# Kernel optimization log

Measured on AMD Instinct MI355X. Metric: run time of the kernel, lower is better.

The kernel has to match this reference:

```python
import jax, jax.numpy as jnp
import numpy as np

B = 1_048_576
NUM_ITERS = 10  # training-mode default; eval mode uses 1000
EPS = 1e-12
LOW, HIGH = 0.02, 0.98  # SquashedSigmoid bounds


def setup_inputs() -> dict:
    key = jax.random.key(0)
    ks = jax.random.split(key, 4)
    # margins are population masses -> keep strictly positive
    margins = jax.random.uniform(ks[0], (B, 8), dtype=jnp.float32) + 0.1

    def lin(k, i, o):
        return (jax.random.normal(k, (i, o), jnp.float32) / np.sqrt(i)).astype(jnp.float32)

    return {
        "margins": margins,
        "W1": lin(ks[1], 8, 32), "b1": jnp.zeros((32,), jnp.float32),
        "W2": lin(ks[2], 32, 16), "b2": jnp.zeros((16,), jnp.float32),
        "W3": lin(ks[3], 16, 9), "b3": jnp.zeros((9,), jnp.float32),
    }


def tau_batched(p):
    # p: (B,4) positive params -> (B,3,3) positive couples matrix.
    # 2x2 core, extended by geometric-mean row/col (user-supplied tau in repo).
    a = p.reshape(-1, 2, 2)
    col3 = jnp.sqrt(a[:, :, 0] * a[:, :, 1])          # (B,2)
    row3 = jnp.sqrt(a[:, 0, :] * a[:, 1, :])          # (B,2)
    corner = jnp.sqrt(row3[:, 0] * row3[:, 1])        # (B,)
    top = jnp.concatenate([a, col3[:, :, None]], axis=2)                 # (B,2,3)
    bot = jnp.concatenate([row3, corner[:, None]], axis=1)[:, None, :]   # (B,1,3)
    return jnp.concatenate([top, bot], axis=1)        # (B,3,3)


def sinkhorn_knopp(A, row_margins, col_margins, iters):
    # Batched Sinkhorn-Knopp: A (B,R,C), row_margins (B,R), col_margins (B,C)
    r = row_margins[:, :, None]
    c = col_margins[:, None, :]

    def body(A, _):
        A = A * (r / (A.sum(axis=2, keepdims=True) + EPS))
        A = A * (c / (A.sum(axis=1, keepdims=True) + EPS))
        return A, None

    A, _ = jax.lax.scan(body, A, None, length=iters)
    return A


def reference(margins, W1, b1, W2, b2, W3, b3):
    Bn = margins.shape[0]
    M, F = margins[:, 0:3], margins[:, 3:6]

    # MLP: Linear-ReLU-Linear-ReLU-Linear
    h = jax.nn.relu(margins @ W1 + b1)
    h = jax.nn.relu(h @ W2 + b2)
    pars = h @ W3 + b3                                   # (B,9)

    muc = tau_batched(jnp.exp(pars[:, 0:4]))             # (B,3,3)
    sqs = lambda x: LOW + (HIGH - LOW) * jax.nn.sigmoid(x)
    shm, shf = sqs(pars[:, 4:6]), sqs(pars[:, 6:8])      # (B,2) each
    V = jnp.exp(pars[:, -1])                             # (B,)

    ones = jnp.ones((Bn, 1), margins.dtype)
    shm0 = jnp.concatenate([shm, ones], axis=1)          # (B,3)
    shf0 = jnp.concatenate([shf, ones], axis=1)          # (B,3)
    mucm0, muc0f = M * shm0, F * shf0                    # matched masses (margins)
    mum0, mu0f = M * (1.0 - shm0), F * (1.0 - shf0)      # singles

    muc = sinkhorn_knopp(muc, mucm0, muc0f, NUM_ITERS)   # (B,3,3)

    top = jnp.concatenate([muc, mum0[:, :, None]], axis=2)   # (B,3,4)
    bot = jnp.concatenate(
        [mu0f[:, None, :], jnp.zeros((Bn, 1, 1), margins.dtype)], axis=2)  # (B,1,4)
    mus = jnp.concatenate([top, bot], axis=1)            # (B,4,4)
    return mus, V
```

## Files before the change

kernel.cpp:

```cpp
#include <hip/hip_runtime.h>
#include <math.h>


#define QLOW  0.02f
#define QSPAN 0.96f
#define L2E   1.44269504088896f

constexpr int R = 2;

typedef __attribute__((ext_vector_type(2))) float f32x2;

__device__ __forceinline__ float frcp(float x) { return __builtin_amdgcn_rcpf(x); }
__device__ __forceinline__ f32x2 pfma(f32x2 a, f32x2 b, f32x2 c) {
    return __builtin_elementwise_fma(a, b, c);
}

__global__ __launch_bounds__(256) void sinkhorn_fused(
    const float* __restrict__ margins,
    const float* __restrict__ W1, const float* __restrict__ b1,
    const float* __restrict__ W2, const float* __restrict__ b2,
    const float* __restrict__ W3, const float* __restrict__ b3,
    float* __restrict__ out, int n)
{
    const int tid  = blockIdx.x * blockDim.x + threadIdx.x;
    const int lane = tid & 63;
    const int base = (tid >> 6) * (64 * R) + lane;

    const float4* __restrict__ m4 = (const float4*)margins;

    float m[R][8];
#pragma unroll
    for (int r = 0; r < R; ++r) {
        const int row = base + 64 * r;
        const float4 a0 = m4[row * 2 + 0];
        const float4 a1 = m4[row * 2 + 1];
        m[r][0] = a0.x; m[r][1] = a0.y; m[r][2] = a0.z; m[r][3] = a0.w;
        m[r][4] = a1.x; m[r][5] = a1.y; m[r][6] = a1.z; m[r][7] = a1.w;
    }

    const f32x2* __restrict__ W1v = (const f32x2*)W1;
    const f32x2* __restrict__ W2v = (const f32x2*)W2;
    const f32x2* __restrict__ b1v = (const f32x2*)b1;
    const f32x2* __restrict__ b2v = (const f32x2*)b2;

    f32x2 h1[R][16];
#pragma unroll
    for (int j = 0; j < 16; ++j) {
        const f32x2 bb = b1v[j];
#pragma unroll
        for (int r = 0; r < R; ++r) h1[r][j] = bb;
    }
#pragma unroll
    for (int k = 0; k < 8; ++k) {
        f32x2 mk[R];
#pragma unroll
        for (int r = 0; r < R; ++r) { mk[r].x = m[r][k]; mk[r].y = m[r][k]; }
#pragma unroll
        for (int j = 0; j < 16; ++j) {
            const f32x2 w = W1v[k * 16 + j];
#pragma unroll
            for (int r = 0; r < R; ++r) h1[r][j] = pfma(mk[r], w, h1[r][j]);
        }
    }
    const f32x2 zero2 = {0.0f, 0.0f};
#pragma unroll
    for (int j = 0; j < 16; ++j)
#pragma unroll
        for (int r = 0; r < R; ++r)
            h1[r][j] = __builtin_elementwise_max(h1[r][j], zero2);

    f32x2 h2[R][8];
#pragma unroll
    for (int j = 0; j < 8; ++j) {
        const f32x2 bb = b2v[j];
#pragma unroll
        for (int r = 0; r < R; ++r) h2[r][j] = bb;
    }
#pragma unroll
    for (int k = 0; k < 32; ++k) {
        f32x2 hk[R];
#pragma unroll
        for (int r = 0; r < R; ++r) {
            const float s = (k & 1) ? h1[r][k >> 1].y : h1[r][k >> 1].x;
            hk[r].x = s; hk[r].y = s;
        }
#pragma unroll
        for (int j = 0; j < 8; ++j) {
            const f32x2 w = W2v[k * 8 + j];
#pragma unroll
            for (int r = 0; r < R; ++r) h2[r][j] = pfma(hk[r], w, h2[r][j]);
        }
    }
#pragma unroll
    for (int j = 0; j < 8; ++j)
#pragma unroll
        for (int r = 0; r < R; ++r)
            h2[r][j] = __builtin_elementwise_max(h2[r][j], zero2);

    f32x2 p01[R], p23[R], p45[R], p67[R];
    float p8[R];
    {
        const f32x2 b01 = {b3[0], b3[1]};
        const f32x2 b23 = {b3[2], b3[3]};
        const f32x2 b45 = {b3[4], b3[5]};
        const f32x2 b67 = {b3[6], b3[7]};
        const float b8  = b3[8];
#pragma unroll
        for (int r = 0; r < R; ++r) {
            p01[r] = b01; p23[r] = b23; p45[r] = b45; p67[r] = b67; p8[r] = b8;
        }
    }
#pragma unroll
    for (int k = 0; k < 16; ++k) {
        const f32x2 w01 = {W3[k * 9 + 0], W3[k * 9 + 1]};
        const f32x2 w23 = {W3[k * 9 + 2], W3[k * 9 + 3]};
        const f32x2 w45 = {W3[k * 9 + 4], W3[k * 9 + 5]};
        const f32x2 w67 = {W3[k * 9 + 6], W3[k * 9 + 7]};
        const float w8  = W3[k * 9 + 8];
#pragma unroll
        for (int r = 0; r < R; ++r) {
            const float s = (k & 1) ? h2[r][k >> 1].y : h2[r][k >> 1].x;
            f32x2 hb; hb.x = s; hb.y = s;
            p01[r] = pfma(hb, w01, p01[r]);
            p23[r] = pfma(hb, w23, p23[r]);
            p45[r] = pfma(hb, w45, p45[r]);
            p67[r] = pfma(hb, w67, p67[r]);
            p8[r]  = fmaf(s, w8, p8[r]);
        }
    }

    float4* __restrict__ o4 = (float4*)out;
    float* __restrict__ oV = out + (size_t)n * 16;

#pragma unroll
    for (int r = 0; r < R; ++r) {
        const int row = base + 64 * r;

        const float l0 = p01[r].x * L2E, l1 = p01[r].y * L2E;
        const float l2 = p23[r].x * L2E, l3 = p23[r].y * L2E;

        const float a00 = exp2f(l0), a01 = exp2f(l1);
        const float a10 = exp2f(l2), a11 = exp2f(l3);
        const float h01 = (l0 + l1) * 0.5f, h23 = (l2 + l3) * 0.5f;
        const float a02 = exp2f(h01);
        const float a12 = exp2f(h23);
        const float a20 = exp2f((l0 + l2) * 0.5f);
        const float a21 = exp2f((l1 + l3) * 0.5f);
        const float a22 = exp2f((h01 + h23) * 0.5f);

        const float s4 = fmaf(QSPAN, frcp(1.0f + exp2f(-L2E * p45[r].x)), QLOW);
        const float s5 = fmaf(QSPAN, frcp(1.0f + exp2f(-L2E * p45[r].y)), QLOW);
        const float s6 = fmaf(QSPAN, frcp(1.0f + exp2f(-L2E * p67[r].x)), QLOW);
        const float s7 = fmaf(QSPAN, frcp(1.0f + exp2f(-L2E * p67[r].y)), QLOW);

        const float M0 = m[r][0], M1 = m[r][1], M2 = m[r][2];
        const float F0 = m[r][3], F1 = m[r][4], F2 = m[r][5];

        const float rm0 = M0 * s4, rm1 = M1 * s5, rm2 = M2;
        const float cm0 = F0 * s6, cm1 = F1 * s7, cm2 = F2;
        const float um0 = fmaf(-s4, M0, M0);
        const float um1 = fmaf(-s5, M1, M1);
        const float uf0 = fmaf(-s6, F0, F0);
        const float uf1 = fmaf(-s7, F1, F1);

        const float B00 = a00 * rm0, B01 = a01 * rm0, B02 = a02 * rm0;
        const float B10 = a10 * rm1, B11 = a11 * rm1, B12 = a12 * rm1;
        const float B20 = a20 * rm2, B21 = a21 * rm2, B22 = a22 * rm2;
        const float C00 = a00 * cm0, C01 = a01 * cm1, C02 = a02 * cm2;
        const float C10 = a10 * cm0, C11 = a11 * cm1, C12 = a12 * cm2;
        const float C20 = a20 * cm0, C21 = a21 * cm1, C22 = a22 * cm2;

        float t0 = (a00 + a01) + a02;
        float t1 = (a10 + a11) + a12;
        float t2 = (a20 + a21) + a22;
        float z0, z1, z2, w0, w1, w2;
#pragma unroll
        for (int it = 0; it < 10; ++it) {
            z0 = frcp(t0); z1 = frcp(t1); z2 = frcp(t2);
            const float q0 = fmaf(B20, z2, fmaf(B10, z1, B00 * z0));
            const float q1 = fmaf(B21, z2, fmaf(B11, z1, B01 * z0));
            const float q2 = fmaf(B22, z2, fmaf(B12, z1, B02 * z0));
            w0 = frcp(q0); w1 = frcp(q1); w2 = frcp(q2);
            if (it < 9) {
                t0 = fmaf(C02, w2, fmaf(C01, w1, C00 * w0));
                t1 = fmaf(C12, w2, fmaf(C11, w1, C10 * w0));
                t2 = fmaf(C22, w2, fmaf(C21, w1, C20 * w0));
            }
        }
        const float u0 = rm0 * z0, u1 = rm1 * z1, u2 = rm2 * z2;
        const float v0 = cm0 * w0, v1 = cm1 * w1, v2 = cm2 * w2;

        const float A0f = u0 * a00 * v0, A1f = u0 * a01 * v1, A2f = u0 * a02 * v2;
        const float A3f = u1 * a10 * v0, A4f = u1 * a11 * v1, A5f = u1 * a12 * v2;
        const float A6f = u2 * a20 * v0, A7f = u2 * a21 * v1, A8f = u2 * a22 * v2;

        o4[row * 4 + 0] = make_float4(A0f, A1f, A2f, um0);
        o4[row * 4 + 1] = make_float4(A3f, A4f, A5f, um1);
        o4[row * 4 + 2] = make_float4(A6f, A7f, A8f, 0.0f);
        o4[row * 4 + 3] = make_float4(uf0, uf1, 0.0f, 0.0f);
        oV[row] = exp2f(p8[r] * L2E);
    }
}

extern "C" void kernel_launch(void* const* d_in, const int* in_sizes, int n_in,
                              void* d_out, int out_size, void* d_ws, size_t ws_size,
                              hipStream_t stream) {
    const float* margins = (const float*)d_in[0];
    const float* W1 = (const float*)d_in[1];
    const float* b1 = (const float*)d_in[2];
    const float* W2 = (const float*)d_in[3];
    const float* b2 = (const float*)d_in[4];
    const float* W3 = (const float*)d_in[5];
    const float* b3 = (const float*)d_in[6];

    const int n = in_sizes[0] / 8;
    const int threads = n / R;
    dim3 block(256), grid(threads / 256);

    sinkhorn_fused<<<grid, block, 0, stream>>>(margins, W1, b1, W2, b2, W3, b3,
                                               (float*)d_out, n);
}
```

Measured before the change: 126.5 us.

## Stage MLP weights in LDS and process one row per thread

Each block now copies W1, W2, W3 and the biases into shared memory, with W3 padded to 12-wide rows so it can be read with float4 LDS loads. The two-rows-per-thread register tiling is dropped in favour of one row per thread, which doubles the grid and lowers register pressure to raise occupancy. The final product also reuses the precomputed C coefficients instead of recomputing v. This trades scalar or global loads of uniform weights for LDS broadcast reads plus a barrier, and gives up the reuse of each weight load across two rows.

```diff
diff --git a/kernel.cpp b/kernel.cpp
--- a/kernel.cpp
+++ b/kernel.cpp
@@ -5,8 +5,6 @@
 #define QLOW  0.02f
 #define QSPAN 0.96f
 #define L2E   1.44269504088896f
-
-constexpr int R = 2;
 
 typedef __attribute__((ext_vector_type(2))) float f32x2;
 
@@ -22,184 +20,160 @@
     const float* __restrict__ W3, const float* __restrict__ b3,
     float* __restrict__ out, int n)
 {
-    const int tid  = blockIdx.x * blockDim.x + threadIdx.x;
-    const int lane = tid & 63;
-    const int base = (tid >> 6) * (64 * R) + lane;
+    __shared__ __align__(16) float sW1[256];
+    __shared__ __align__(16) float sW2[512];
+    __shared__ __align__(16) float sW3[16 * 12];
+    __shared__ __align__(16) float sB1[32];
+    __shared__ __align__(16) float sB2[16];
+    __shared__ __align__(16) float sB3[12];
+
+    {
+        const int t = threadIdx.x;
+        sW1[t] = W1[t];
+        sW2[t] = W2[t];
+        sW2[t + 256] = W2[t + 256];
+        if (t < 144) { const int k = t / 9, j = t - 9 * k; sW3[k * 12 + j] = W3[t]; }
+        if (t < 32) sB1[t] = b1[t];
+        if (t < 16) sB2[t] = b2[t];
+        if (t < 9)  sB3[t] = b3[t];
+    }
+    __syncthreads();
+
+    const float4* __restrict__ sW1q = (const float4*)sW1;
+    const float4* __restrict__ sW2q = (const float4*)sW2;
+    const float4* __restrict__ sW3q = (const float4*)sW3;
+
+    const int row = blockIdx.x * blockDim.x + threadIdx.x;
 
     const float4* __restrict__ m4 = (const float4*)margins;
+    const float4 a0 = m4[row * 2 + 0];
+    const float4 a1 = m4[row * 2 + 1];
+    float m[8];
+    m[0] = a0.x; m[1] = a0.y; m[2] = a0.z; m[3] = a0.w;
+    m[4] = a1.x; m[5] = a1.y; m[6] = a1.z; m[7] = a1.w;
 
-    float m[R][8];
+    f32x2 h1[16];
 #pragma unroll
-    for (int r = 0; r < R; ++r) {
-        const int row = base + 64 * r;
-        const float4 a0 = m4[row * 2 + 0];
-        const float4 a1 = m4[row * 2 + 1];
-        m[r][0] = a0.x; m[r][1] = a0.y; m[r][2] = a0.z; m[r][3] = a0.w;
-        m[r][4] = a1.x; m[r][5] = a1.y; m[r][6] = a1.z; m[r][7] = a1.w;
-    }
-
-    const f32x2* __restrict__ W1v = (const f32x2*)W1;
-    const f32x2* __restrict__ W2v = (const f32x2*)W2;
-    const f32x2* __restrict__ b1v = (const f32x2*)b1;
-    const f32x2* __restrict__ b2v = (const f32x2*)b2;
-
-    f32x2 h1[R][16];
-#pragma unroll
-    for (int j = 0; j < 16; ++j) {
-        const f32x2 bb = b1v[j];
-#pragma unroll
-        for (int r = 0; r < R; ++r) h1[r][j] = bb;
-    }
+    for (int j = 0; j < 16; ++j) { h1[j].x = sB1[2 * j]; h1[j].y = sB1[2 * j + 1]; }
 #pragma unroll
     for (int k = 0; k < 8; ++k) {
-        f32x2 mk[R];
+        f32x2 mk; mk.x = m[k]; mk.y = m[k];
 #pragma unroll
-        for (int r = 0; r < R; ++r) { mk[r].x = m[r][k]; mk[r].y = m[r][k]; }
-#pragma unroll
-        for (int j = 0; j < 16; ++j) {
-            const f32x2 w = W1v[k * 16 + j];
-#pragma unroll
-            for (int r = 0; r < R; ++r) h1[r][j] = pfma(mk[r], w, h1[r][j]);
+        for (int j4 = 0; j4 < 8; ++j4) {
+            const float4 w = sW1q[k * 8 + j4];
+            const f32x2 wa = {w.x, w.y};
+            const f32x2 wb = {w.z, w.w};
+            h1[2 * j4 + 0] = pfma(mk, wa, h1[2 * j4 + 0]);
+            h1[2 * j4 + 1] = pfma(mk, wb, h1[2 * j4 + 1]);
         }
     }
     const f32x2 zero2 = {0.0f, 0.0f};
 #pragma unroll
-    for (int j = 0; j < 16; ++j)
+    for (int j = 0; j < 16; ++j) h1[j] = __builtin_elementwise_max(h1[j], zero2);
+
+    f32x2 h2[8];
 #pragma unroll
-        for (int r = 0; r < R; ++r)
-            h1[r][j] = __builtin_elementwise_max(h1[r][j], zero2);
-
-    f32x2 h2[R][8];
-#pragma unroll
-    for (int j = 0; j < 8; ++j) {
-        const f32x2 bb = b2v[j];
-#pragma unroll
-        for (int r = 0; r < R; ++r) h2[r][j] = bb;
-    }
+    for (int j = 0; j < 8; ++j) { h2[j].x = sB2[2 * j]; h2[j].y = sB2[2 * j + 1]; }
 #pragma unroll
     for (int k = 0; k < 32; ++k) {
-        f32x2 hk[R];
+        const float s = (k & 1) ? h1[k >> 1].y : h1[k >> 1].x;
+        f32x2 hk; hk.x = s; hk.y = s;
 #pragma unroll
-        for (int r = 0; r < R; ++r) {
-            const float s = (k & 1) ? h1[r][k >> 1].y : h1[r][k >> 1].x;
-            hk[r].x = s; hk[r].y = s;
-        }
-#pragma unroll
-        for (int j = 0; j < 8; ++j) {
-            const f32x2 w = W2v[k * 8 + j];
-#pragma unroll
-            for (int r = 0; r < R; ++r) h2[r][j] = pfma(hk[r], w, h2[r][j]);
+        for (int j4 = 0; j4 < 4; ++j4) {
+            const float4 w = sW2q[k * 4 + j4];
+            const f32x2 wa = {w.x, w.y};
+            const f32x2 wb = {w.z, w.w};
+            h2[2 * j4 + 0] = pfma(hk, wa, h2[2 * j4 + 0]);
+            h2[2 * j4 + 1] = pfma(hk, wb, h2[2 * j4 + 1]);
         }
     }
 #pragma unroll
-    for (int j = 0; j < 8; ++j)
+    for (int j = 0; j < 8; ++j) h2[j] = __builtin_elementwise_max(h2[j], zero2);
+
+    f32x2 p01 = {sB3[0], sB3[1]};
+    f32x2 p23 = {sB3[2], sB3[3]};
+    f32x2 p45 = {sB3[4], sB3[5]};
+    f32x2 p67 = {sB3[6], sB3[7]};
+    float p8 = sB3[8];
 #pragma unroll
-        for (int r = 0; r < R; ++r)
-            h2[r][j] = __builtin_elementwise_max(h2[r][j], zero2);
+    for (int k = 0; k < 16; ++k) {
+        const float4 wA = sW3q[k * 3 + 0];
+        const float4 wB = sW3q[k * 3 + 1];
+        const float w8  = sW3[k * 12 + 8];
+        const float s = (k & 1) ? h2[k >> 1].y : h2[k >> 1].x;
+        f32x2 hb; hb.x = s; hb.y = s;
+        p01 = pfma(hb, (f32x2){wA.x, wA.y}, p01);
+        p23 = pfma(hb, (f32x2){wA.z, wA.w}, p23);
+        p45 = pfma(hb, (f32x2){wB.x, wB.y}, p45);
+        p67 = pfma(hb, (f32x2){wB.z, wB.w}, p67);
+        p8  = fmaf(s, w8, p8);
+    }
 
-    f32x2 p01[R], p23[R], p45[R], p67[R];
-    float p8[R];
-    {
-        const f32x2 b01 = {b3[0], b3[1]};
-        const f32x2 b23 = {b3[2], b3[3]};
-        const f32x2 b45 = {b3[4], b3[5]};
-        const f32x2 b67 = {b3[6], b3[7]};
-        const float b8  = b3[8];
+    const float l0 = p01.x * L2E, l1 = p01.y * L2E;
+    const float l2 = p23.x * L2E, l3 = p23.y * L2E;
+
+    const float a00 = exp2f(l0), a01 = exp2f(l1);
+    const float a10 = exp2f(l2), a11 = exp2f(l3);
+    const float h01 = (l0 + l1) * 0.5f, h23 = (l2 + l3) * 0.5f;
+    const float a02 = exp2f(h01);
+    const float a12 = exp2f(h23);
+    const float a20 = exp2f((l0 + l2) * 0.5f);
+    const float a21 = exp2f((l1 + l3) * 0.5f);
+    const float a22 = exp2f((h01 + h23) * 0.5f);
+
+    const float s4 = fmaf(QSPAN, frcp(1.0f + exp2f(-L2E * p45.x)), QLOW);
+    const float s5 = fmaf(QSPAN, frcp(1.0f + exp2f(-L2E * p45.y)), QLOW);
+    const float s6 = fmaf(QSPAN, frcp(1.0f + exp2f(-L2E * p67.x)), QLOW);
+    const float s7 = fmaf(QSPAN, frcp(1.0f + exp2f(-L2E * p67.y)), QLOW);
+
+    const float M0 = m[0], M1 = m[1], M2 = m[2];
+    const float F0 = m[3], F1 = m[4], F2 = m[5];
+
+    const float rm0 = M0 * s4, rm1 = M1 * s5, rm2 = M2;
+    const float cm0 = F0 * s6, cm1 = F1 * s7, cm2 = F2;
+    const float um0 = fmaf(-s4, M0, M0);
+    const float um1 = fmaf(-s5, M1, M1);
+    const float uf0 = fmaf(-s6, F0, F0);
+    const float uf1 = fmaf(-s7, F1, F1);
+
+    const float B00 = a00 * rm0, B01 = a01 * rm0, B02 = a02 * rm0;
+    const float B10 = a10 * rm1, B11 = a11 * rm1, B12 = a12 * rm1;
+    const float B20 = a20 * rm2, B21 = a21 * rm2, B22 = a22 * rm2;
+    const float C00 = a00 * cm0, C01 = a01 * cm1, C02 = a02 * cm2;
+    const float C10 = a10 * cm0, C11 = a11 * cm1, C12 = a12 * cm2;
+    const float C20 = a20 * cm0, C21 = a21 * cm1, C22 = a22 * cm2;
+
+    float t0 = (a00 + a01) + a02;
+    float t1 = (a10 + a11) + a12;
+    float t2 = (a20 + a21) + a22;
+    float z0, z1, z2, w0, w1, w2;
 #pragma unroll
-        for (int r = 0; r < R; ++r) {
-            p01[r] = b01; p23[r] = b23; p45[r] = b45; p67[r] = b67; p8[r] = b8;
+    for (int it = 0; it < 10; ++it) {
+        z0 = frcp(t0); z1 = frcp(t1); z2 = frcp(t2);
+        const float q0 = fmaf(B20, z2, fmaf(B10, z1, B00 * z0));
+        const float q1 = fmaf(B21, z2, fmaf(B11, z1, B01 * z0));
+        const float q2 = fmaf(B22, z2, fmaf(B12, z1, B02 * z0));
+        w0 = frcp(q0); w1 = frcp(q1); w2 = frcp(q2);
+        if (it < 9) {
+            t0 = fmaf(C02, w2, fmaf(C01, w1, C00 * w0));
+            t1 = fmaf(C12, w2, fmaf(C11, w1, C10 * w0));
+            t2 = fmaf(C22, w2, fmaf(C21, w1, C20 * w0));
         }
     }
-#pragma unroll
-    for (int k = 0; k < 16; ++k) {
-        const f32x2 w01 = {W3[k * 9 + 0], W3[k * 9 + 1]};
-        const f32x2 w23 = {W3[k * 9 + 2], W3[k * 9 + 3]};
-        const f32x2 w45 = {W3[k * 9 + 4], W3[k * 9 + 5]};
-        const f32x2 w67 = {W3[k * 9 + 6], W3[k * 9 + 7]};
-        const float w8  = W3[k * 9 + 8];
-#pragma unroll
-        for (int r = 0; r < R; ++r) {
-            const float s = (k & 1) ? h2[r][k >> 1].y : h2[r][k >> 1].x;
-            f32x2 hb; hb.x = s; hb.y = s;
-            p01[r] = pfma(hb, w01, p01[r]);
-            p23[r] = pfma(hb, w23, p23[r]);
-            p45[r] = pfma(hb, w45, p45[r]);
-            p67[r] = pfma(hb, w67, p67[r]);
-            p8[r]  = fmaf(s, w8, p8[r]);
-        }
-    }
+    const float u0 = rm0 * z0, u1 = rm1 * z1, u2 = rm2 * z2;
+
+    const float A0f = u0 * C00 * w0, A1f = u0 * C01 * w1, A2f = u0 * C02 * w2;
+    const float A3f = u1 * C10 * w0, A4f = u1 * C11 * w1, A5f = u1 * C12 * w2;
+    const float A6f = u2 * C20 * w0, A7f = u2 * C21 * w1, A8f = u2 * C22 * w2;
 
     float4* __restrict__ o4 = (float4*)out;
     float* __restrict__ oV = out + (size_t)n * 16;
 
-#pragma unroll
-    for (int r = 0; r < R; ++r) {
-        const int row = base + 64 * r;
-
-        const float l0 = p01[r].x * L2E, l1 = p01[r].y * L2E;
-        const float l2 = p23[r].x * L2E, l3 = p23[r].y * L2E;
-
-        const float a00 = exp2f(l0), a01 = exp2f(l1);
-        const float a10 = exp2f(l2), a11 = exp2f(l3);
-        const float h01 = (l0 + l1) * 0.5f, h23 = (l2 + l3) * 0.5f;
-        const float a02 = exp2f(h01);
-        const float a12 = exp2f(h23);
-        const float a20 = exp2f((l0 + l2) * 0.5f);
-        const float a21 = exp2f((l1 + l3) * 0.5f);
-        const float a22 = exp2f((h01 + h23) * 0.5f);
-
-        const float s4 = fmaf(QSPAN, frcp(1.0f + exp2f(-L2E * p45[r].x)), QLOW);
-        const float s5 = fmaf(QSPAN, frcp(1.0f + exp2f(-L2E * p45[r].y)), QLOW);
-        const float s6 = fmaf(QSPAN, frcp(1.0f + exp2f(-L2E * p67[r].x)), QLOW);
-        const float s7 = fmaf(QSPAN, frcp(1.0f + exp2f(-L2E * p67[r].y)), QLOW);
-
-        const float M0 = m[r][0], M1 = m[r][1], M2 = m[r][2];
-        const float F0 = m[r][3], F1 = m[r][4], F2 = m[r][5];
-
-        const float rm0 = M0 * s4, rm1 = M1 * s5, rm2 = M2;
-        const float cm0 = F0 * s6, cm1 = F1 * s7, cm2 = F2;
-        const float um0 = fmaf(-s4, M0, M0);
-        const float um1 = fmaf(-s5, M1, M1);
-        const float uf0 = fmaf(-s6, F0, F0);
-        const float uf1 = fmaf(-s7, F1, F1);
-
-        const float B00 = a00 * rm0, B01 = a01 * rm0, B02 = a02 * rm0;
-        const float B10 = a10 * rm1, B11 = a11 * rm1, B12 = a12 * rm1;
-        const float B20 = a20 * rm2, B21 = a21 * rm2, B22 = a22 * rm2;
-        const float C00 = a00 * cm0, C01 = a01 * cm1, C02 = a02 * cm2;
-        const float C10 = a10 * cm0, C11 = a11 * cm1, C12 = a12 * cm2;
-        const float C20 = a20 * cm0, C21 = a21 * cm1, C22 = a22 * cm2;
-
-        float t0 = (a00 + a01) + a02;
-        float t1 = (a10 + a11) + a12;
-        float t2 = (a20 + a21) + a22;
-        float z0, z1, z2, w0, w1, w2;
-#pragma unroll
-        for (int it = 0; it < 10; ++it) {
-            z0 = frcp(t0); z1 = frcp(t1); z2 = frcp(t2);
-            const float q0 = fmaf(B20, z2, fmaf(B10, z1, B00 * z0));
-            const float q1 = fmaf(B21, z2, fmaf(B11, z1, B01 * z0));
-            const float q2 = fmaf(B22, z2, fmaf(B12, z1, B02 * z0));
-            w0 = frcp(q0); w1 = frcp(q1); w2 = frcp(q2);
-            if (it < 9) {
-                t0 = fmaf(C02, w2, fmaf(C01, w1, C00 * w0));
-                t1 = fmaf(C12, w2, fmaf(C11, w1, C10 * w0));
-                t2 = fmaf(C22, w2, fmaf(C21, w1, C20 * w0));
-            }
-        }
-        const float u0 = rm0 * z0, u1 = rm1 * z1, u2 = rm2 * z2;
-        const float v0 = cm0 * w0, v1 = cm1 * w1, v2 = cm2 * w2;
-
-        const float A0f = u0 * a00 * v0, A1f = u0 * a01 * v1, A2f = u0 * a02 * v2;
-        const float A3f = u1 * a10 * v0, A4f = u1 * a11 * v1, A5f = u1 * a12 * v2;
-        const float A6f = u2 * a20 * v0, A7f = u2 * a21 * v1, A8f = u2 * a22 * v2;
-
-        o4[row * 4 + 0] = make_float4(A0f, A1f, A2f, um0);
-        o4[row * 4 + 1] = make_float4(A3f, A4f, A5f, um1);
-        o4[row * 4 + 2] = make_float4(A6f, A7f, A8f, 0.0f);
-        o4[row * 4 + 3] = make_float4(uf0, uf1, 0.0f, 0.0f);
-        oV[row] = exp2f(p8[r] * L2E);
-    }
+    o4[row * 4 + 0] = make_float4(A0f, A1f, A2f, um0);
+    o4[row * 4 + 1] = make_float4(A3f, A4f, A5f, um1);
+    o4[row * 4 + 2] = make_float4(A6f, A7f, A8f, 0.0f);
+    o4[row * 4 + 3] = make_float4(uf0, uf1, 0.0f, 0.0f);
+    oV[row] = exp2f(p8 * L2E);
 }
 
 extern "C" void kernel_launch(void* const* d_in, const int* in_sizes, int n_in,
@@ -214,8 +188,7 @@
     const float* b3 = (const float*)d_in[6];
 
     const int n = in_sizes[0] / 8;
-    const int threads = n / R;
-    dim3 block(256), grid(threads / 256);
+    dim3 block(256), grid(n / 256);
 
     sinkhorn_fused<<<grid, block, 0, stream>>>(margins, W1, b1, W2, b2, W3, b3,
                                                (float*)d_out, n);
```

Result: slower. 136.9 us (+8.3%).
